# Optimization experiments

Hardware: AMD Instinct MI355X
Metric: run time of the kernel (lower is better)

Reference implementation:

```python
import jax, jax.numpy as jnp
import numpy as np

B, N = 8, 2048
IN_DIM, MEM_DIM, CTX_DIM = 256, 256, 128

def _linear_params(key, out_dim, in_dim):
    kw, kb = jax.random.split(key)
    bound = 1.0 / np.sqrt(in_dim)
    W = jax.random.uniform(kw, (out_dim, in_dim), jnp.float32, -bound, bound)
    b = jax.random.uniform(kb, (out_dim,), jnp.float32, -bound, bound)
    return W, b

def setup_inputs() -> dict:
    key = jax.random.key(0)
    ks = jax.random.split(key, 8)
    Wq, bq = _linear_params(ks[0], CTX_DIM, IN_DIM)
    Wk, bk = _linear_params(ks[1], CTX_DIM, MEM_DIM)
    Wv, bv = _linear_params(ks[2], MEM_DIM, MEM_DIM)
    Wu, bu = _linear_params(ks[3], MEM_DIM, IN_DIM + MEM_DIM)
    Wr, br = _linear_params(ks[4], MEM_DIM, IN_DIM + MEM_DIM)
    Wc, bc = _linear_params(ks[5], MEM_DIM, IN_DIM + MEM_DIM)
    input_tensor = jax.random.normal(ks[6], (B, N, IN_DIM), jnp.float32)
    previous_memory = jax.random.normal(ks[7], (B, N, MEM_DIM), jnp.float32)
    return dict(input_tensor=input_tensor, previous_memory=previous_memory,
                Wq=Wq, bq=bq, Wk=Wk, bk=bk, Wv=Wv, bv=bv,
                Wu=Wu, bu=bu, Wr=Wr, br=br, Wc=Wc, bc=bc)

def reference(input_tensor, previous_memory, Wq, bq, Wk, bk, Wv, bv, Wu, bu, Wr, br, Wc, bc):
    # QKV projections (torch Linear: y = x @ W.T + b)
    query = jnp.einsum('bnd,cd->bnc', input_tensor, Wq) + bq        # [B,N,CTX]
    key = jnp.einsum('bnm,cm->bnc', previous_memory, Wk) + bk       # [B,N,CTX]
    value = jnp.einsum('bnm,vm->bnv', previous_memory, Wv) + bv     # [B,N,MEM]
    attention_scores = jnp.einsum('bqc,bkc->bqk', query, key)        # [B,N,N]
    attention_probs = jax.nn.softmax(attention_scores, axis=-1)
    context_vector = jnp.einsum('bqk,bkv->bqv', attention_probs, value)  # computed but unused downstream, as in original
    combined = jnp.concatenate([input_tensor, previous_memory], axis=-1)  # [B,N,IN+MEM]
    update_gate = jax.nn.sigmoid(jnp.einsum('bnd,md->bnm', combined, Wu) + bu)
    reset_gate = jax.nn.sigmoid(jnp.einsum('bnd,md->bnm', combined, Wr) + br)
    cand_in = jnp.concatenate([input_tensor, reset_gate * previous_memory], axis=-1)
    candidate_memory = jnp.tanh(jnp.einsum('bnd,md->bnm', cand_in, Wc) + bc)
    new_memory = (1.0 - update_gate) * previous_memory + update_gate * candidate_memory
    return new_memory, attention_probs
```

## Files before the change

### kernel.cpp

```cpp
#include <hip/hip_runtime.h>
#include <hip/hip_cooperative_groups.h>

namespace cg = cooperative_groups;


typedef _Float16 half8 __attribute__((ext_vector_type(8)));
typedef _Float16 half4 __attribute__((ext_vector_type(4)));
typedef float floatx4 __attribute__((ext_vector_type(4)));

#define MFMA16(a, b, c) __builtin_amdgcn_mfma_f32_16x16x32_f16((a), (b), (c), 0, 0, 0)

#define OFF_Q   524288
#define OFF_K   2621440

__device__ __forceinline__ void gload16(const void* g, void* l) {
  __builtin_amdgcn_global_load_lds((const __attribute__((address_space(1))) unsigned int*)g,
                                   (__attribute__((address_space(3))) unsigned int*)l, 16, 0, 0);
}


__device__ __forceinline__ void role_k2ru(
    char* smem, int job, int tid,
    const float* __restrict__ input, const float* __restrict__ prev,
    const float* __restrict__ Wr, const float* __restrict__ br,
    const float* __restrict__ Wu, const float* __restrict__ bu,
    _Float16* __restrict__ t_sc, _Float16* __restrict__ u_sc)
{
  const int w = tid >> 6, l = tid & 63;
  const int lr = l & 15, lg = l >> 4;
  const int rows0 = (job & 127) * 128;
  const int isU = w >> 2;
  const int c = (job >> 7) * 64 + (w & 3) * 16 + lr;

  const float* Wf = isU ? Wu : Wr;
  half8 bw[16];
#pragma unroll
  for (int ks = 0; ks < 16; ++ks) {
    floatx4 w0 = *(const floatx4*)(Wf + (size_t)c * 512 + ks * 32 + lg * 8);
    floatx4 w1 = *(const floatx4*)(Wf + (size_t)c * 512 + ks * 32 + lg * 8 + 4);
    half8 h;
#pragma unroll
    for (int j = 0; j < 4; ++j) { h[j] = (_Float16)w0[j]; h[4 + j] = (_Float16)w1[j]; }
    bw[ks] = h;
  }
  const float bv = (isU ? bu : br)[c];

  const int srow = tid >> 5, scol = (tid & 31) * 8;
  const int ssz = (srow & 7) << 4;
  floatx4 sI0, sI1, sP0, sP1;

#define K2RU_LOAD(ch) { \
  const float* si = input + ((size_t)rows0 + (ch) * 16 + srow) * 256 + scol; \
  const float* sp = prev  + ((size_t)rows0 + (ch) * 16 + srow) * 256 + scol; \
  sI0 = *(const floatx4*)si; sI1 = *(const floatx4*)(si + 4); \
  sP0 = *(const floatx4*)sp; sP1 = *(const floatx4*)(sp + 4); }
#define K2RU_WRITE(ch) { char* bufw = smem + ((ch) & 1) * 16384; \
  half8 hi, hp; \
  _Pragma("unroll") for (int j = 0; j < 4; ++j) { \
    hi[j] = (_Float16)sI0[j]; hi[4+j] = (_Float16)sI1[j]; \
    hp[j] = (_Float16)sP0[j]; hp[4+j] = (_Float16)sP1[j]; } \
  int o = srow * 1024 + ((scol * 2) ^ ssz); \
  *(half8*)(bufw + o) = hi; *(half8*)(bufw + o + 512) = hp; }

  K2RU_LOAD(0); K2RU_WRITE(0);
  __syncthreads();
#pragma unroll 1
  for (int ch = 0; ch < 8; ++ch) {
    if (ch < 7) K2RU_LOAD(ch + 1);
    const char* buf = smem + (ch & 1) * 16384;
    floatx4 acc = {0.f, 0.f, 0.f, 0.f};
    const int base = lr * 1024, sz = (lr & 7) << 4;
#pragma unroll
    for (int ks = 0; ks < 16; ++ks) {
      half8 a = *(const half8*)(buf + base + ((ks * 64 + lg * 16) ^ sz));
      acc = MFMA16(a, bw[ks], acc);
    }
#pragma unroll
    for (int j = 0; j < 4; ++j) {
      const int crow = lg * 4 + j;
      const size_t grow = (size_t)rows0 + ch * 16 + crow;
      float g = 1.f / (1.f + __expf(-(acc[j] + bv)));
      if (!isU) {
        float m = (float)*(const _Float16*)(buf + crow * 1024 + 512 + ((c * 2) ^ ((crow & 7) << 4)));
        t_sc[grow * 256 + c] = (_Float16)(g * m);
      } else {
        u_sc[grow * 256 + c] = (_Float16)g;
      }
    }
    if (ch < 7) K2RU_WRITE(ch + 1);
    __syncthreads();
  }
}

__device__ __forceinline__ void role_k1(
    char* smem, int job, int tid,
    const float* __restrict__ input, const float* __restrict__ prev,
    const float* __restrict__ Wq, const float* __restrict__ bq,
    const float* __restrict__ Wk, const float* __restrict__ bk,
    _Float16* __restrict__ ws)
{
  const int w = tid >> 6, l = tid & 63;
  const int lr = l & 15, lg = l >> 4;
  const int which = job >> 8;
  const int rows0 = (job & 255) * 64;
  const float* x = which ? prev : input;
  const float* Wf = which ? Wk : Wq;
  const float* bias = which ? bk : bq;
  _Float16* out = ws + (which ? OFF_K : OFF_Q);
  const int c = w * 16 + lr;

  half8 bh[8], blo[8];
#pragma unroll
  for (int ks = 0; ks < 8; ++ks) {
    floatx4 w0 = *(const floatx4*)(Wf + (size_t)c * 256 + ks * 32 + lg * 8);
    floatx4 w1 = *(const floatx4*)(Wf + (size_t)c * 256 + ks * 32 + lg * 8 + 4);
    half8 h, lo;
#pragma unroll
    for (int j = 0; j < 4; ++j) {
      _Float16 h0 = (_Float16)w0[j];
      h[j] = h0; lo[j] = (_Float16)(w0[j] - (float)h0);
      _Float16 h1 = (_Float16)w1[j];
      h[4 + j] = h1; lo[4 + j] = (_Float16)(w1[j] - (float)h1);
    }
    bh[ks] = h; blo[ks] = lo;
  }
  const float bv = bias[c];

  const int srow = tid >> 5, scol = (tid & 31) * 8;
  const int ssz = (srow & 7) << 4;
  floatx4 st0, st1;

#define K1_LOAD(ch) { const float* src = x + ((size_t)rows0 + (ch) * 16 + srow) * 256 + scol; \
  st0 = *(const floatx4*)src; st1 = *(const floatx4*)(src + 4); }
#define K1_WRITE(ch) { char* bufw = smem + ((ch) & 1) * 8192; \
  half8 h; \
  _Pragma("unroll") for (int j = 0; j < 4; ++j) { \
    h[j] = (_Float16)st0[j]; h[4+j] = (_Float16)st1[j]; } \
  *(half8*)(bufw + srow * 512 + ((scol * 2) ^ ssz)) = h; }

  K1_LOAD(0); K1_WRITE(0);
  __syncthreads();
#pragma unroll 1
  for (int ch = 0; ch < 4; ++ch) {
    if (ch < 3) K1_LOAD(ch + 1);
    const char* buf = smem + (ch & 1) * 8192;
    floatx4 acc = {0.f, 0.f, 0.f, 0.f};
    const int base = lr * 512, sz = (lr & 7) << 4;
#pragma unroll
    for (int ks = 0; ks < 8; ++ks) {
      half8 ah = *(const half8*)(buf + base + ((ks * 64 + lg * 16) ^ sz));
      acc = MFMA16(ah, bh[ks], acc);
      acc = MFMA16(ah, blo[ks], acc);
    }
#pragma unroll
    for (int j = 0; j < 4; ++j)
      out[((size_t)rows0 + ch * 16 + lg * 4 + j) * 128 + c] = (_Float16)(acc[j] + bv);
    if (ch < 3) K1_WRITE(ch + 1);
    __syncthreads();
  }
}

#define K3_STAGE(Kg, dst, ch) { \
  const char* g_ = (Kg) + (ch) * 32768; \
  _Pragma("unroll") for (int i_ = 0; i_ < 4; ++i_) { \
    int o_ = w * 1024 + i_ * 8192 + l * 16; \
    int row_ = o_ >> 8, col_ = o_ & 255; \
    gload16(g_ + row_ * 256 + (col_ ^ ((row_ & 7) << 4)), (dst) + w * 1024 + i_ * 8192); } }

__device__ __forceinline__ void role_k3a(
    char* smem, int job, int tid,
    const _Float16* __restrict__ ws, float* __restrict__ part)
{
  const int w = tid >> 6, l = tid & 63;
  const int lr = l & 15, lg = l >> 4;
  const int b = job & 7, q0 = ((job >> 3) & 15) * 128, kh = job >> 7;

  const _Float16* Q = ws + OFF_Q + ((size_t)b * 2048 + q0 + w * 16) * 128;
  const char* Kg = (const char*)(ws + OFF_K + ((size_t)b * 2048 + kh * 512) * 128);

  half8 qf[4];
#pragma unroll
  for (int ks = 0; ks < 4; ++ks)
    qf[ks] = *(const half8*)(Q + (size_t)lr * 128 + ks * 32 + lg * 8);

  char* kbuf0 = smem; char* kbuf1 = smem + 32768;
  K3_STAGE(Kg, kbuf0, 0);
  __syncthreads();

  float se = 0.f;
#pragma unroll 1
  for (int ch = 0; ch < 4; ++ch) {
    if (ch < 3) K3_STAGE(Kg, ((ch + 1) & 1) ? kbuf1 : kbuf0, ch + 1);
    const char* buf = (ch & 1) ? kbuf1 : kbuf0;
#pragma unroll
    for (int kt = 0; kt < 8; ++kt) {
      const int kk = kt * 16 + lr;
      const int kbase = kk * 256, ksz = (kk & 7) << 4;
      half8 kf[4];
#pragma unroll
      for (int ks = 0; ks < 4; ++ks)
        kf[ks] = *(const half8*)(buf + kbase + ((ks * 64 + lg * 16) ^ ksz));
      floatx4 acc = {0.f, 0.f, 0.f, 0.f};
#pragma unroll
      for (int ks = 0; ks < 4; ++ks) acc = MFMA16(kf[ks], qf[ks], acc);
#pragma unroll
      for (int j = 0; j < 4; ++j) se += __expf(acc[j] - 14.f);
    }
    __syncthreads();
  }
  se += __shfl_xor(se, 16);
  se += __shfl_xor(se, 32);
  if (lg == 0)
    part[((size_t)b * 4 + kh) * 2048 + q0 + w * 16 + lr] = se;
}

__device__ __forceinline__ void role_k2c(
    char* smem, int job, int tid,
    const float* __restrict__ input, const float* __restrict__ prev,
    const float* __restrict__ Wc, const float* __restrict__ bc,
    const _Float16* __restrict__ t_sc, const _Float16* __restrict__ u_sc,
    float* __restrict__ out0)
{
  const int w = tid >> 6, l = tid & 63;
  const int lr = l & 15, lg = l >> 4;
  const int rows0 = (job & 255) * 64;
  const int c = (job >> 8) * 128 + w * 16 + lr;

  half8 bw[16];
#pragma unroll
  for (int ks = 0; ks < 16; ++ks) {
    floatx4 w0 = *(const floatx4*)(Wc + (size_t)c * 512 + ks * 32 + lg * 8);
    floatx4 w1 = *(const floatx4*)(Wc + (size_t)c * 512 + ks * 32 + lg * 8 + 4);
    half8 h;
#pragma unroll
    for (int j = 0; j < 4; ++j) { h[j] = (_Float16)w0[j]; h[4 + j] = (_Float16)w1[j]; }
    bw[ks] = h;
  }
  const float bv = bc[c];

  const int srow = tid >> 5, scol = (tid & 31) * 8;
  const int ssz = (srow & 7) << 4;
  floatx4 sI0, sI1;
  half8 sT;

#define K2C_LOAD(ch) { \
  const float* si = input + ((size_t)rows0 + (ch) * 16 + srow) * 256 + scol; \
  sI0 = *(const floatx4*)si; sI1 = *(const floatx4*)(si + 4); \
  sT = *(const half8*)(t_sc + ((size_t)rows0 + (ch) * 16 + srow) * 256 + scol); }
#define K2C_WRITE(ch) { char* bufw = smem + ((ch) & 1) * 16384; \
  half8 hi; \
  _Pragma("unroll") for (int j = 0; j < 4; ++j) { hi[j] = (_Float16)sI0[j]; hi[4+j] = (_Float16)sI1[j]; } \
  int o = srow * 1024 + ((scol * 2) ^ ssz); \
  *(half8*)(bufw + o) = hi; *(half8*)(bufw + o + 512) = sT; }

  K2C_LOAD(0); K2C_WRITE(0);
  __syncthreads();
#pragma unroll 1
  for (int ch = 0; ch < 4; ++ch) {
    if (ch < 3) K2C_LOAD(ch + 1);
    const char* buf = smem + (ch & 1) * 16384;
    floatx4 acc = {0.f, 0.f, 0.f, 0.f};
    const int base = lr * 1024, sz = (lr & 7) << 4;
#pragma unroll
    for (int ks = 0; ks < 16; ++ks) {
      half8 a = *(const half8*)(buf + base + ((ks * 64 + lg * 16) ^ sz));
      acc = MFMA16(a, bw[ks], acc);
    }
#pragma unroll
    for (int j = 0; j < 4; ++j) {
      const size_t grow = (size_t)rows0 + ch * 16 + lg * 4 + j;
      float e2 = __expf(2.f * (acc[j] + bv));
      float cg = (e2 - 1.f) / (e2 + 1.f);
      float u = (float)u_sc[grow * 256 + c];
      float m = prev[grow * 256 + c];
      out0[grow * 256 + c] = (1.f - u) * m + u * cg;
    }
    if (ch < 3) K2C_WRITE(ch + 1);
    __syncthreads();
  }
}

__device__ __forceinline__ void role_k3b(
    char* smem, int job, int tid,
    const _Float16* __restrict__ ws, const float* __restrict__ part,
    float* __restrict__ out1)
{
  const int w = tid >> 6, l = tid & 63;
  const int lr = l & 15, lg = l >> 4;
  const int b = job & 7, q0 = ((job >> 3) & 15) * 128, kh = job >> 7;

  const int q = q0 + w * 16 + lr;
  const _Float16* Q = ws + OFF_Q + ((size_t)b * 2048 + q0 + w * 16) * 128;
  const char* Kg = (const char*)(ws + OFF_K + ((size_t)b * 2048 + kh * 512) * 128);

  half8 qf[4];
#pragma unroll
  for (int ks = 0; ks < 4; ++ks)
    qf[ks] = *(const half8*)(Q + (size_t)lr * 128 + ks * 32 + lg * 8);
  const float inv = 1.f / (part[(size_t)(b * 4 + 0) * 2048 + q] +
                           part[(size_t)(b * 4 + 1) * 2048 + q] +
                           part[(size_t)(b * 4 + 2) * 2048 + q] +
                           part[(size_t)(b * 4 + 3) * 2048 + q]);

  char* kbuf0 = smem; char* kbuf1 = smem + 32768;
  K3_STAGE(Kg, kbuf0, 0);
  __syncthreads();

  float* orow = out1 + ((size_t)b * 2048 + q) * 2048 + kh * 512;
#pragma unroll 1
  for (int ch = 0; ch < 4; ++ch) {
    if (ch < 3) K3_STAGE(Kg, ((ch + 1) & 1) ? kbuf1 : kbuf0, ch + 1);
    const char* buf = (ch & 1) ? kbuf1 : kbuf0;
#pragma unroll
    for (int kt = 0; kt < 8; ++kt) {
      const int kk = kt * 16 + lr;
      const int kbase = kk * 256, ksz = (kk & 7) << 4;
      half8 kf[4];
#pragma unroll
      for (int ks = 0; ks < 4; ++ks)
        kf[ks] = *(const half8*)(buf + kbase + ((ks * 64 + lg * 16) ^ ksz));
      floatx4 acc = {0.f, 0.f, 0.f, 0.f};
#pragma unroll
      for (int ks = 0; ks < 4; ++ks) acc = MFMA16(kf[ks], qf[ks], acc);
      floatx4 v;
#pragma unroll
      for (int j = 0; j < 4; ++j) v[j] = __expf(acc[j] - 14.f) * inv;
      *(floatx4*)(orow + ch * 128 + kt * 16 + lg * 4) = v;
    }
    __syncthreads();
  }
}

__global__ __launch_bounds__(512, 4) void mega(
    const float* __restrict__ input, const float* __restrict__ prev,
    const float* __restrict__ Wq, const float* __restrict__ bq,
    const float* __restrict__ Wk, const float* __restrict__ bk,
    const float* __restrict__ Wr, const float* __restrict__ br,
    const float* __restrict__ Wu, const float* __restrict__ bu,
    const float* __restrict__ Wc, const float* __restrict__ bc,
    _Float16* __restrict__ ws, float* __restrict__ part,
    _Float16* __restrict__ t_sc, _Float16* __restrict__ u_sc,
    float* __restrict__ out0, float* __restrict__ out1)
{
  __shared__ char smem[65536];
  cg::grid_group grid = cg::this_grid();
  const int bid = blockIdx.x, tid = threadIdx.x;

  role_k2ru(smem, bid, tid, input, prev, Wr, br, Wu, bu, t_sc, u_sc);
  __syncthreads();
  role_k1(smem, bid, tid, input, prev, Wq, bq, Wk, bk, ws);
  grid.sync();

  role_k3a(smem, bid, tid, ws, part);
  __syncthreads();
  role_k2c(smem, bid, tid, input, prev, Wc, bc, t_sc, u_sc, out0);
  grid.sync();

  role_k3b(smem, bid, tid, ws, part, out1);
}

__global__ __launch_bounds__(512, 4) void kA_fb(
    const float* __restrict__ input, const float* __restrict__ prev,
    const float* __restrict__ Wq, const float* __restrict__ bq,
    const float* __restrict__ Wk, const float* __restrict__ bk,
    const float* __restrict__ Wr, const float* __restrict__ br,
    const float* __restrict__ Wu, const float* __restrict__ bu,
    _Float16* __restrict__ ws,
    _Float16* __restrict__ t_sc, _Float16* __restrict__ u_sc)
{
  __shared__ char smem[32768];
  if (blockIdx.x < 512)
    role_k2ru(smem, blockIdx.x, threadIdx.x, input, prev, Wr, br, Wu, bu, t_sc, u_sc);
  else
    role_k1(smem, blockIdx.x - 512, threadIdx.x, input, prev, Wq, bq, Wk, bk, ws);
}

__global__ __launch_bounds__(512, 4) void kB_fb(
    const float* __restrict__ input, const float* __restrict__ prev,
    const float* __restrict__ Wc, const float* __restrict__ bc,
    const _Float16* __restrict__ ws, float* __restrict__ part,
    const _Float16* __restrict__ t_sc, const _Float16* __restrict__ u_sc,
    float* __restrict__ out0)
{
  __shared__ char smem[65536];
  if (blockIdx.x < 512)
    role_k3a(smem, blockIdx.x, threadIdx.x, ws, part);
  else
    role_k2c(smem, blockIdx.x - 512, threadIdx.x, input, prev, Wc, bc, t_sc, u_sc, out0);
}

__global__ __launch_bounds__(512, 4) void kC_fb(
    const _Float16* __restrict__ ws, const float* __restrict__ part,
    float* __restrict__ out1)
{
  __shared__ char smem[65536];
  role_k3b(smem, blockIdx.x, threadIdx.x, ws, part, out1);
}

extern "C" void kernel_launch(void* const* d_in, const int* in_sizes, int n_in,
                              void* d_out, int out_size, void* d_ws, size_t ws_size,
                              hipStream_t stream)
{
  const float* input = (const float*)d_in[0];
  const float* prev  = (const float*)d_in[1];
  const float* Wq = (const float*)d_in[2];
  const float* bq = (const float*)d_in[3];
  const float* Wk = (const float*)d_in[4];
  const float* bk = (const float*)d_in[5];
  const float* Wu = (const float*)d_in[8];
  const float* bu = (const float*)d_in[9];
  const float* Wr = (const float*)d_in[10];
  const float* br = (const float*)d_in[11];
  const float* Wc = (const float*)d_in[12];
  const float* bc = (const float*)d_in[13];

  float* out0 = (float*)d_out;
  float* out1 = out0 + (size_t)8 * 2048 * 256;
  _Float16* ws = (_Float16*)d_ws;

  _Float16* t_sc = (_Float16*)out1;
  _Float16* u_sc = (_Float16*)out1 + 4194304;
  float* part = (float*)ws;

  int occ = 0;
  hipOccupancyMaxActiveBlocksPerMultiprocessor(&occ, (const void*)mega, 512, 0);

  if (occ >= 2) {
    void* args[] = { (void*)&input, (void*)&prev, (void*)&Wq, (void*)&bq,
                     (void*)&Wk, (void*)&bk, (void*)&Wr, (void*)&br,
                     (void*)&Wu, (void*)&bu, (void*)&Wc, (void*)&bc,
                     (void*)&ws, (void*)&part, (void*)&t_sc, (void*)&u_sc,
                     (void*)&out0, (void*)&out1 };
    hipLaunchCooperativeKernel((void*)mega, dim3(512), dim3(512), args, 0, stream);
  } else {
    hipLaunchKernelGGL(kA_fb, dim3(1024), dim3(512), 0, stream,
                       input, prev, Wq, bq, Wk, bk, Wr, br, Wu, bu, ws, t_sc, u_sc);
    hipLaunchKernelGGL(kB_fb, dim3(1024), dim3(512), 0, stream,
                       input, prev, Wc, bc, ws, part, t_sc, u_sc, out0);
    hipLaunchKernelGGL(kC_fb, dim3(512), dim3(512), 0, stream, ws, part, out1);
  }
}
```

Baseline: 111.0 us.

## Replace cooperative mega-kernel with staged launches and pre-split QK weights

Drops the cooperative kernel that used grid.sync and replaces it with a sequence of normal launches. A tiny kernel first splits Wq/Wk into fp16 hi/lo parts, then a projection kernel writes Q/K. When the workspace is large enough, a kernel runs the reset/update gates alongside the softmax row-sum pass, and a final kernel runs the probability write alongside the candidate/new-memory pass, with t/u scratch moved into the workspace. The aim is to avoid grid-wide barrier cost and rebalance how work from different stages shares the GPU, at the cost of extra launches and intermediate round-trips through global memory.

Result: faster. 107.2 us (-3.5%).

```diff
diff --git a/kernel.cpp b/kernel.cpp
--- a/kernel.cpp
+++ b/kernel.cpp
@@ -1,23 +1,103 @@
 #include <hip/hip_runtime.h>
-#include <hip/hip_cooperative_groups.h>
-
-namespace cg = cooperative_groups;
 
 
 typedef _Float16 half8 __attribute__((ext_vector_type(8)));
-typedef _Float16 half4 __attribute__((ext_vector_type(4)));
 typedef float floatx4 __attribute__((ext_vector_type(4)));
 
 #define MFMA16(a, b, c) __builtin_amdgcn_mfma_f32_16x16x32_f16((a), (b), (c), 0, 0, 0)
 
+#define OFF_WQH 0
+#define OFF_WQL 32768
+#define OFF_WKH 65536
+#define OFF_WKL 98304
 #define OFF_Q   524288
 #define OFF_K   2621440
+#define OFF_T   4718592
+#define OFF_U   8912896
 
 __device__ __forceinline__ void gload16(const void* g, void* l) {
   __builtin_amdgcn_global_load_lds((const __attribute__((address_space(1))) unsigned int*)g,
                                    (__attribute__((address_space(3))) unsigned int*)l, 16, 0, 0);
 }
 
+__global__ __launch_bounds__(256) void k0qk(
+    const float* __restrict__ Wq, const float* __restrict__ Wk,
+    _Float16* __restrict__ ws)
+{
+  int i = blockIdx.x * 256 + threadIdx.x;
+  if (i < 32768) {
+    float w = Wq[i];
+    _Float16 h = (_Float16)w;
+    ws[OFF_WQH + i] = h;
+    ws[OFF_WQL + i] = (_Float16)(w - (float)h);
+  } else {
+    int j = i - 32768;
+    float w = Wk[j];
+    _Float16 h = (_Float16)w;
+    ws[OFF_WKH + j] = h;
+    ws[OFF_WKL + j] = (_Float16)(w - (float)h);
+  }
+}
+
+__global__ __launch_bounds__(512) void k1_proj(
+    const float* __restrict__ input, const float* __restrict__ prev,
+    const float* __restrict__ bq, const float* __restrict__ bk,
+    _Float16* __restrict__ ws)
+{
+  __shared__ char smem[2 * 8192];
+  const int which = blockIdx.y;
+  const float* x = which ? prev : input;
+  const _Float16* WH = ws + (which ? OFF_WKH : OFF_WQH);
+  const _Float16* WL = ws + (which ? OFF_WKL : OFF_WQL);
+  const float* bias = which ? bk : bq;
+  _Float16* out = ws + (which ? OFF_K : OFF_Q);
+
+  const int tid = threadIdx.x, w = tid >> 6, l = tid & 63;
+  const int lr = l & 15, lg = l >> 4;
+  const int rows0 = blockIdx.x * 64;
+  const int c = w * 16 + lr;
+
+  half8 bh[8], blo[8];
+#pragma unroll
+  for (int ks = 0; ks < 8; ++ks) {
+    bh[ks]  = *(const half8*)(WH + (size_t)c * 256 + ks * 32 + lg * 8);
+    blo[ks] = *(const half8*)(WL + (size_t)c * 256 + ks * 32 + lg * 8);
+  }
+  const float bv = bias[c];
+
+  const int srow = tid >> 5, scol = (tid & 31) * 8;
+  const int ssz = (srow & 7) << 4;
+  floatx4 st0, st1;
+
+#define K1_LOAD(ch) { const float* src = x + ((size_t)rows0 + (ch) * 16 + srow) * 256 + scol; \
+  st0 = *(const floatx4*)src; st1 = *(const floatx4*)(src + 4); }
+#define K1_WRITE(ch) { char* bufw = smem + ((ch) & 1) * 8192; \
+  half8 h; \
+  _Pragma("unroll") for (int j = 0; j < 4; ++j) { \
+    h[j] = (_Float16)st0[j]; h[4+j] = (_Float16)st1[j]; } \
+  *(half8*)(bufw + srow * 512 + ((scol * 2) ^ ssz)) = h; }
+
+  K1_LOAD(0); K1_WRITE(0);
+  __syncthreads();
+#pragma unroll 1
+  for (int ch = 0; ch < 4; ++ch) {
+    if (ch < 3) K1_LOAD(ch + 1);
+    const char* buf = smem + (ch & 1) * 8192;
+    floatx4 acc = {0.f, 0.f, 0.f, 0.f};
+    const int base = lr * 512, sz = (lr & 7) << 4;
+#pragma unroll
+    for (int ks = 0; ks < 8; ++ks) {
+      half8 ah = *(const half8*)(buf + base + ((ks * 64 + lg * 16) ^ sz));
+      acc = MFMA16(ah, bh[ks], acc);
+      acc = MFMA16(ah, blo[ks], acc);
+    }
+#pragma unroll
+    for (int j = 0; j < 4; ++j)
+      out[((size_t)rows0 + ch * 16 + lg * 4 + j) * 128 + c] = (_Float16)(acc[j] + bv);
+    if (ch < 3) K1_WRITE(ch + 1);
+    __syncthreads();
+  }
+}
 
 __device__ __forceinline__ void role_k2ru(
     char* smem, int job, int tid,
@@ -92,74 +172,6 @@
   }
 }
 
-__device__ __forceinline__ void role_k1(
-    char* smem, int job, int tid,
-    const float* __restrict__ input, const float* __restrict__ prev,
-    const float* __restrict__ Wq, const float* __restrict__ bq,
-    const float* __restrict__ Wk, const float* __restrict__ bk,
-    _Float16* __restrict__ ws)
-{
-  const int w = tid >> 6, l = tid & 63;
-  const int lr = l & 15, lg = l >> 4;
-  const int which = job >> 8;
-  const int rows0 = (job & 255) * 64;
-  const float* x = which ? prev : input;
-  const float* Wf = which ? Wk : Wq;
-  const float* bias = which ? bk : bq;
-  _Float16* out = ws + (which ? OFF_K : OFF_Q);
-  const int c = w * 16 + lr;
-
-  half8 bh[8], blo[8];
-#pragma unroll
-  for (int ks = 0; ks < 8; ++ks) {
-    floatx4 w0 = *(const floatx4*)(Wf + (size_t)c * 256 + ks * 32 + lg * 8);
-    floatx4 w1 = *(const floatx4*)(Wf + (size_t)c * 256 + ks * 32 + lg * 8 + 4);
-    half8 h, lo;
-#pragma unroll
-    for (int j = 0; j < 4; ++j) {
-      _Float16 h0 = (_Float16)w0[j];
-      h[j] = h0; lo[j] = (_Float16)(w0[j] - (float)h0);
-      _Float16 h1 = (_Float16)w1[j];
-      h[4 + j] = h1; lo[4 + j] = (_Float16)(w1[j] - (float)h1);
-    }
-    bh[ks] = h; blo[ks] = lo;
-  }
-  const float bv = bias[c];
-
-  const int srow = tid >> 5, scol = (tid & 31) * 8;
-  const int ssz = (srow & 7) << 4;
-  floatx4 st0, st1;
-
-#define K1_LOAD(ch) { const float* src = x + ((size_t)rows0 + (ch) * 16 + srow) * 256 + scol; \
-  st0 = *(const floatx4*)src; st1 = *(const floatx4*)(src + 4); }
-#define K1_WRITE(ch) { char* bufw = smem + ((ch) & 1) * 8192; \
-  half8 h; \
-  _Pragma("unroll") for (int j = 0; j < 4; ++j) { \
-    h[j] = (_Float16)st0[j]; h[4+j] = (_Float16)st1[j]; } \
-  *(half8*)(bufw + srow * 512 + ((scol * 2) ^ ssz)) = h; }
-
-  K1_LOAD(0); K1_WRITE(0);
-  __syncthreads();
-#pragma unroll 1
-  for (int ch = 0; ch < 4; ++ch) {
-    if (ch < 3) K1_LOAD(ch + 1);
-    const char* buf = smem + (ch & 1) * 8192;
-    floatx4 acc = {0.f, 0.f, 0.f, 0.f};
-    const int base = lr * 512, sz = (lr & 7) << 4;
-#pragma unroll
-    for (int ks = 0; ks < 8; ++ks) {
-      half8 ah = *(const half8*)(buf + base + ((ks * 64 + lg * 16) ^ sz));
-      acc = MFMA16(ah, bh[ks], acc);
-      acc = MFMA16(ah, blo[ks], acc);
-    }
-#pragma unroll
-    for (int j = 0; j < 4; ++j)
-      out[((size_t)rows0 + ch * 16 + lg * 4 + j) * 128 + c] = (_Float16)(acc[j] + bv);
-    if (ch < 3) K1_WRITE(ch + 1);
-    __syncthreads();
-  }
-}
-
 #define K3_STAGE(Kg, dst, ch) { \
   const char* g_ = (Kg) + (ch) * 32768; \
   _Pragma("unroll") for (int i_ = 0; i_ < 4; ++i_) { \
@@ -214,8 +226,59 @@
     part[((size_t)b * 4 + kh) * 2048 + q0 + w * 16 + lr] = se;
 }
 
+__device__ __forceinline__ void role_k3b(
+    char* smem, int job, int tid,
+    const _Float16* __restrict__ ws, const float* __restrict__ part,
+    float* __restrict__ out1)
+{
+  const int w = tid >> 6, l = tid & 63;
+  const int lr = l & 15, lg = l >> 4;
+  const int b = job & 7, q0 = ((job >> 3) & 15) * 128, kh = job >> 7;
+
+  const int q = q0 + w * 16 + lr;
+  const _Float16* Q = ws + OFF_Q + ((size_t)b * 2048 + q0 + w * 16) * 128;
+  const char* Kg = (const char*)(ws + OFF_K + ((size_t)b * 2048 + kh * 512) * 128);
+
+  half8 qf[4];
+#pragma unroll
+  for (int ks = 0; ks < 4; ++ks)
+    qf[ks] = *(const half8*)(Q + (size_t)lr * 128 + ks * 32 + lg * 8);
+  const float inv = 1.f / (part[(size_t)(b * 4 + 0) * 2048 + q] +
+                           part[(size_t)(b * 4 + 1) * 2048 + q] +
+                           part[(size_t)(b * 4 + 2) * 2048 + q] +
+                           part[(size_t)(b * 4 + 3) * 2048 + q]);
+
+  char* kbuf0 = smem; char* kbuf1 = smem + 32768;
+  K3_STAGE(Kg, kbuf0, 0);
+  __syncthreads();
+
+  float* orow = out1 + ((size_t)b * 2048 + q) * 2048 + kh * 512;
+#pragma unroll 1
+  for (int ch = 0; ch < 4; ++ch) {
+    if (ch < 3) K3_STAGE(Kg, ((ch + 1) & 1) ? kbuf1 : kbuf0, ch + 1);
+    const char* buf = (ch & 1) ? kbuf1 : kbuf0;
+#pragma unroll
+    for (int kt = 0; kt < 8; ++kt) {
+      const int kk = kt * 16 + lr;
+      const int kbase = kk * 256, ksz = (kk & 7) << 4;
+      half8 kf[4];
+#pragma unroll
+      for (int ks = 0; ks < 4; ++ks)
+        kf[ks] = *(const half8*)(buf + kbase + ((ks * 64 + lg * 16) ^ ksz));
+      floatx4 acc = {0.f, 0.f, 0.f, 0.f};
+#pragma unroll
+      for (int ks = 0; ks < 4; ++ks) acc = MFMA16(kf[ks], qf[ks], acc);
+      floatx4 v;
+#pragma unroll
+      for (int j = 0; j < 4; ++j) v[j] = __expf(acc[j] - 14.f) * inv;
+      *(floatx4*)(orow + ch * 128 + kt * 16 + lg * 4) = v;
+    }
+    __syncthreads();
+  }
+}
+
 __device__ __forceinline__ void role_k2c(
-    char* smem, int job, int tid,
+    char* smemc, int job, int tid,
     const float* __restrict__ input, const float* __restrict__ prev,
     const float* __restrict__ Wc, const float* __restrict__ bc,
     const _Float16* __restrict__ t_sc, const _Float16* __restrict__ u_sc,
@@ -247,7 +310,7 @@
   const float* si = input + ((size_t)rows0 + (ch) * 16 + srow) * 256 + scol; \
   sI0 = *(const floatx4*)si; sI1 = *(const floatx4*)(si + 4); \
   sT = *(const half8*)(t_sc + ((size_t)rows0 + (ch) * 16 + srow) * 256 + scol); }
-#define K2C_WRITE(ch) { char* bufw = smem + ((ch) & 1) * 16384; \
+#define K2C_WRITE(ch) { char* bufw = smemc + ((ch) & 1) * 16384; \
   half8 hi; \
   _Pragma("unroll") for (int j = 0; j < 4; ++j) { hi[j] = (_Float16)sI0[j]; hi[4+j] = (_Float16)sI1[j]; } \
   int o = srow * 1024 + ((scol * 2) ^ ssz); \
@@ -258,7 +321,7 @@
 #pragma unroll 1
   for (int ch = 0; ch < 4; ++ch) {
     if (ch < 3) K2C_LOAD(ch + 1);
-    const char* buf = smem + (ch & 1) * 16384;
+    const char* buf = smemc + (ch & 1) * 16384;
     floatx4 acc = {0.f, 0.f, 0.f, 0.f};
     const int base = lr * 1024, sz = (lr & 7) << 4;
 #pragma unroll
@@ -280,121 +343,67 @@
   }
 }
 
-__device__ __forceinline__ void role_k3b(
-    char* smem, int job, int tid,
-    const _Float16* __restrict__ ws, const float* __restrict__ part,
-    float* __restrict__ out1)
-{
-  const int w = tid >> 6, l = tid & 63;
-  const int lr = l & 15, lg = l >> 4;
-  const int b = job & 7, q0 = ((job >> 3) & 15) * 128, kh = job >> 7;
-
-  const int q = q0 + w * 16 + lr;
-  const _Float16* Q = ws + OFF_Q + ((size_t)b * 2048 + q0 + w * 16) * 128;
-  const char* Kg = (const char*)(ws + OFF_K + ((size_t)b * 2048 + kh * 512) * 128);
-
-  half8 qf[4];
-#pragma unroll
-  for (int ks = 0; ks < 4; ++ks)
-    qf[ks] = *(const half8*)(Q + (size_t)lr * 128 + ks * 32 + lg * 8);
-  const float inv = 1.f / (part[(size_t)(b * 4 + 0) * 2048 + q] +
-                           part[(size_t)(b * 4 + 1) * 2048 + q] +
-                           part[(size_t)(b * 4 + 2) * 2048 + q] +
-                           part[(size_t)(b * 4 + 3) * 2048 + q]);
-
-  char* kbuf0 = smem; char* kbuf1 = smem + 32768;
-  K3_STAGE(Kg, kbuf0, 0);
-  __syncthreads();
-
-  float* orow = out1 + ((size_t)b * 2048 + q) * 2048 + kh * 512;
-#pragma unroll 1
-  for (int ch = 0; ch < 4; ++ch) {
-    if (ch < 3) K3_STAGE(Kg, ((ch + 1) & 1) ? kbuf1 : kbuf0, ch + 1);
-    const char* buf = (ch & 1) ? kbuf1 : kbuf0;
-#pragma unroll
-    for (int kt = 0; kt < 8; ++kt) {
-      const int kk = kt * 16 + lr;
-      const int kbase = kk * 256, ksz = (kk & 7) << 4;
-      half8 kf[4];
-#pragma unroll
-      for (int ks = 0; ks < 4; ++ks)
-        kf[ks] = *(const half8*)(buf + kbase + ((ks * 64 + lg * 16) ^ ksz));
-      floatx4 acc = {0.f, 0.f, 0.f, 0.f};
-#pragma unroll
-      for (int ks = 0; ks < 4; ++ks) acc = MFMA16(kf[ks], qf[ks], acc);
-      floatx4 v;
-#pragma unroll
-      for (int j = 0; j < 4; ++j) v[j] = __expf(acc[j] - 14.f) * inv;
-      *(floatx4*)(orow + ch * 128 + kt * 16 + lg * 4) = v;
-    }
-    __syncthreads();
-  }
-}
-
-__global__ __launch_bounds__(512, 4) void mega(
-    const float* __restrict__ input, const float* __restrict__ prev,
-    const float* __restrict__ Wq, const float* __restrict__ bq,
-    const float* __restrict__ Wk, const float* __restrict__ bk,
+__global__ __launch_bounds__(512, 4) void kE(
+    const float* __restrict__ input, const float* __restrict__ prev,
     const float* __restrict__ Wr, const float* __restrict__ br,
     const float* __restrict__ Wu, const float* __restrict__ bu,
-    const float* __restrict__ Wc, const float* __restrict__ bc,
-    _Float16* __restrict__ ws, float* __restrict__ part,
-    _Float16* __restrict__ t_sc, _Float16* __restrict__ u_sc,
-    float* __restrict__ out0, float* __restrict__ out1)
+    const _Float16* __restrict__ ws, float* __restrict__ part,
+    _Float16* __restrict__ t_sc, _Float16* __restrict__ u_sc)
 {
   __shared__ char smem[65536];
-  cg::grid_group grid = cg::this_grid();
-  const int bid = blockIdx.x, tid = threadIdx.x;
-
-  role_k2ru(smem, bid, tid, input, prev, Wr, br, Wu, bu, t_sc, u_sc);
-  __syncthreads();
-  role_k1(smem, bid, tid, input, prev, Wq, bq, Wk, bk, ws);
-  grid.sync();
-
-  role_k3a(smem, bid, tid, ws, part);
-  __syncthreads();
-  role_k2c(smem, bid, tid, input, prev, Wc, bc, t_sc, u_sc, out0);
-  grid.sync();
-
-  role_k3b(smem, bid, tid, ws, part, out1);
-}
-
-__global__ __launch_bounds__(512, 4) void kA_fb(
-    const float* __restrict__ input, const float* __restrict__ prev,
-    const float* __restrict__ Wq, const float* __restrict__ bq,
-    const float* __restrict__ Wk, const float* __restrict__ bk,
-    const float* __restrict__ Wr, const float* __restrict__ br,
-    const float* __restrict__ Wu, const float* __restrict__ bu,
-    _Float16* __restrict__ ws,
-    _Float16* __restrict__ t_sc, _Float16* __restrict__ u_sc)
-{
-  __shared__ char smem[32768];
   if (blockIdx.x < 512)
     role_k2ru(smem, blockIdx.x, threadIdx.x, input, prev, Wr, br, Wu, bu, t_sc, u_sc);
   else
-    role_k1(smem, blockIdx.x - 512, threadIdx.x, input, prev, Wq, bq, Wk, bk, ws);
-}
-
-__global__ __launch_bounds__(512, 4) void kB_fb(
+    role_k3a(smem, blockIdx.x - 512, threadIdx.x, ws, part);
+}
+
+__global__ __launch_bounds__(512, 4) void kD(
     const float* __restrict__ input, const float* __restrict__ prev,
     const float* __restrict__ Wc, const float* __restrict__ bc,
-    const _Float16* __restrict__ ws, float* __restrict__ part,
+    const _Float16* __restrict__ ws, const float* __restrict__ part,
+    const _Float16* __restrict__ t_sc, const _Float16* __restrict__ u_sc,
+    float* __restrict__ out0, float* __restrict__ out1)
+{
+  __shared__ char smem[65536];
+  if (blockIdx.x < 512)
+    role_k3b(smem, blockIdx.x, threadIdx.x, ws, part, out1);
+  else
+    role_k2c(smem, blockIdx.x - 512, threadIdx.x, input, prev, Wc, bc, t_sc, u_sc, out0);
+}
+
+__global__ __launch_bounds__(512) void k2ru_kernel(
+    const float* __restrict__ input, const float* __restrict__ prev,
+    const float* __restrict__ Wr, const float* __restrict__ br,
+    const float* __restrict__ Wu, const float* __restrict__ bu,
+    _Float16* __restrict__ t_sc, _Float16* __restrict__ u_sc)
+{
+  __shared__ char smem[32768];
+  role_k2ru(smem, blockIdx.x, threadIdx.x, input, prev, Wr, br, Wu, bu, t_sc, u_sc);
+}
+
+__global__ __launch_bounds__(512) void k3a_kernel(
+    const _Float16* __restrict__ ws, float* __restrict__ part)
+{
+  __shared__ char smem[65536];
+  role_k3a(smem, blockIdx.x, threadIdx.x, ws, part);
+}
+
+__global__ __launch_bounds__(512) void k3b_kernel(
+    const _Float16* __restrict__ ws, const float* __restrict__ part,
+    float* __restrict__ out1)
+{
+  __shared__ char smem[65536];
+  role_k3b(smem, blockIdx.x, threadIdx.x, ws, part, out1);
+}
+
+__global__ __launch_bounds__(512) void k2c_kernel(
+    const float* __restrict__ input, const float* __restrict__ prev,
+    const float* __restrict__ Wc, const float* __restrict__ bc,
     const _Float16* __restrict__ t_sc, const _Float16* __restrict__ u_sc,
     float* __restrict__ out0)
 {
-  __shared__ char smem[65536];
-  if (blockIdx.x < 512)
-    role_k3a(smem, blockIdx.x, threadIdx.x, ws, part);
-  else
-    role_k2c(smem, blockIdx.x - 512, threadIdx.x, input, prev, Wc, bc, t_sc, u_sc, out0);
-}
-
-__global__ __launch_bounds__(512, 4) void kC_fb(
-    const _Float16* __restrict__ ws, const float* __restrict__ part,
-    float* __restrict__ out1)
-{
-  __shared__ char smem[65536];
-  role_k3b(smem, blockIdx.x, threadIdx.x, ws, part, out1);
+  __shared__ char smemc[32768];
+  role_k2c(smemc, blockIdx.x, threadIdx.x, input, prev, Wc, bc, t_sc, u_sc, out0);
 }
 
 extern "C" void kernel_launch(void* const* d_in, const int* in_sizes, int n_in,
@@ -418,25 +427,27 @@
   float* out1 = out0 + (size_t)8 * 2048 * 256;
   _Float16* ws = (_Float16*)d_ws;
 
-  _Float16* t_sc = (_Float16*)out1;
-  _Float16* u_sc = (_Float16*)out1 + 4194304;
   float* part = (float*)ws;
-
-  int occ = 0;
-  hipOccupancyMaxActiveBlocksPerMultiprocessor(&occ, (const void*)mega, 512, 0);
-
-  if (occ >= 2) {
-    void* args[] = { (void*)&input, (void*)&prev, (void*)&Wq, (void*)&bq,
-                     (void*)&Wk, (void*)&bk, (void*)&Wr, (void*)&br,
-                     (void*)&Wu, (void*)&bu, (void*)&Wc, (void*)&bc,
-                     (void*)&ws, (void*)&part, (void*)&t_sc, (void*)&u_sc,
-                     (void*)&out0, (void*)&out1 };
-    hipLaunchCooperativeKernel((void*)mega, dim3(512), dim3(512), args, 0, stream);
+  const bool big = ws_size >= (size_t)26214400;
+
+  hipLaunchKernelGGL(k0qk,    dim3(256), dim3(256), 0, stream, Wq, Wk, ws);
+  hipLaunchKernelGGL(k1_proj, dim3(256, 2), dim3(512), 0, stream, input, prev, bq, bk, ws);
+
+  if (big) {
+    _Float16* t_sc = ws + OFF_T;
+    _Float16* u_sc = ws + OFF_U;
+    hipLaunchKernelGGL(kE, dim3(1024), dim3(512), 0, stream,
+                       input, prev, Wr, br, Wu, bu, ws, part, t_sc, u_sc);
+    hipLaunchKernelGGL(kD, dim3(1024), dim3(512), 0, stream,
+                       input, prev, Wc, bc, ws, part, t_sc, u_sc, out0, out1);
   } else {
-    hipLaunchKernelGGL(kA_fb, dim3(1024), dim3(512), 0, stream,
-                       input, prev, Wq, bq, Wk, bk, Wr, br, Wu, bu, ws, t_sc, u_sc);
-    hipLaunchKernelGGL(kB_fb, dim3(1024), dim3(512), 0, stream,
-                       input, prev, Wc, bc, ws, part, t_sc, u_sc, out0);
-    hipLaunchKernelGGL(kC_fb, dim3(512), dim3(512), 0, stream, ws, part, out1);
-  }
-}
+    _Float16* t_sc = (_Float16*)out1;
+    _Float16* u_sc = (_Float16*)out1 + 4194304;
+    hipLaunchKernelGGL(k2ru_kernel, dim3(512), dim3(512), 0, stream,
+                       input, prev, Wr, br, Wu, bu, t_sc, u_sc);
+    hipLaunchKernelGGL(k2c_kernel,  dim3(512), dim3(512), 0, stream,
+                       input, prev, Wc, bc, t_sc, u_sc, out0);
+    hipLaunchKernelGGL(k3a_kernel,  dim3(512), dim3(512), 0, stream, ws, part);
+    hipLaunchKernelGGL(k3b_kernel,  dim3(512), dim3(512), 0, stream, ws, part, out1);
+  }
+}
```
